# Performance work log

Measured on AMD Instinct MI355X. Metric: run time of the kernel, lower is better.

Reference implementation:

```python
import jax, jax.numpy as jnp
import numpy as np

B, L, A = 16, 32, 2046
M = A + 2  # user col + attributors + item col = 2048 nodes


def _xavier_uniform(key, shape, gain):
    fan_out, fan_in = shape  # torch 2D param: fan_in = shape[1], fan_out = shape[0]
    bound = gain * np.sqrt(6.0 / (fan_in + fan_out))
    return jax.random.uniform(key, shape, jnp.float32, -bound, bound)


def setup_inputs() -> dict:
    key = jax.random.key(0)
    k = jax.random.split(key, 7)
    user = jax.random.normal(k[0], (B, 6 * L, 1), jnp.float32)
    item = jax.random.normal(k[1], (B, 6 * L, 1), jnp.float32)
    attributor = jax.random.normal(k[2], (B, 6 * L, A), jnp.float32)
    adj = (jax.random.uniform(k[3], (M, M)) < 0.5).astype(jnp.float32)
    initial_weight = jax.random.normal(k[4], (M, M), jnp.float32)
    W_1 = _xavier_uniform(k[5], (6 * L, A), gain=np.sqrt(2.0))  # relu gain
    W_2 = _xavier_uniform(k[6], (6 * L, L), gain=1.44)
    return {"user": user, "item": item, "attributor": attributor,
            "adj": adj, "initial_weight": initial_weight,
            "W_1": W_1, "W_2": W_2}


def reference(user, item, attributor, adj, initial_weight, W_1, W_2):
    N = W_2.shape[1]  # = length L
    a = attributor * W_1                                   # (B, 6L, A)
    raw = jnp.concatenate([user, a, item], axis=2)         # (B, 6L, M)
    Q, K, V = jnp.split(raw, 3, axis=1)                    # each (B, 2L, M)
    r = jax.nn.relu
    # (relu(X).T @ W).T  ==  einsum over the 2L dim -> (B, L, M)
    Query = jnp.einsum('bnm,nl->blm', r(Q), W_2[:2 * N])
    Key = jnp.einsum('bnm,nl->blm', r(K), W_2[2 * N:4 * N])
    Value = jnp.einsum('bnm,nl->blm', r(V), W_2[4 * N:])
    # h = Query.mT @ Key * adj * initial_weight  -> (B, M, M)
    h = jnp.einsum('blm,bln->bmn', Query, Key) * adj * initial_weight
    d = h - jnp.swapaxes(h, -1, -2)
    exp_h = jnp.exp(jnp.where(d > 0, 0.0, d))              # exp(min(d, 0))
    causal = exp_h / (exp_h + jnp.swapaxes(exp_h, -1, -2)) * adj  # (B, M, M)
    Ans = Value @ causal                                    # (B, L, M)
    idx = jnp.array([0, Ans.shape[2] - 1])
    return Ans[:, :, idx]                                   # (B, L, 2)
```

## Files before the change

kernel.cpp:

```cpp
#include <hip/hip_runtime.h>
#include <math.h>

#define BB 16
#define LL 32
#define AA 2046
#define MM 2048
#define NROWS 192


__global__ __launch_bounds__(256) void prep_kernel(
    const float* __restrict__ user, const float* __restrict__ item,
    const float* __restrict__ W2, float* __restrict__ uv,
    float* __restrict__ bnd) {
  const int b = blockIdx.x, t = threadIdx.x;
  __shared__ float KQ[4][LL];
  __shared__ float uvs[4][64];
  if (t < 128) {
    const int q = t >> 5, l = t & 31;
    const float* __restrict__ src = (q & 1) ? item : user;
    const int rbase = (q < 2) ? 64 : 0;
    float acc = 0.f;
#pragma unroll
    for (int r = 0; r < 64; ++r)
      acc += fmaxf(src[b * NROWS + rbase + r], 0.f) * W2[(rbase + r) * LL + l];
    KQ[q][l] = acc;
  }
  __syncthreads();
  {
    const int which = t >> 6, r = t & 63;
    const int wrow = (which < 2) ? r : 64 + r;
    float acc = 0.f;
#pragma unroll
    for (int l = 0; l < LL; ++l) acc += W2[wrow * LL + l] * KQ[which][l];
    uvs[which][r] = acc;
    uv[which * (BB * 64) + b * 64 + r] = acc;
  }
  __syncthreads();
  if (t < 8) {
    const int which = t & 1, j = (t >> 1) & 1, stv = t >> 2;
    const float* __restrict__ src = which ? item : user;
    float acc = 0.f;
    if (stv == 0) {
#pragma unroll
      for (int r = 0; r < 64; ++r)
        acc += fmaxf(src[b * NROWS + r], 0.f) * uvs[j][r];
    } else {
#pragma unroll
      for (int r = 0; r < 64; ++r)
        acc += fmaxf(src[b * NROWS + 64 + r], 0.f) * uvs[2 + j][r];
    }
    bnd[((j * 2 + stv) * 2 + which) * BB + b] = acc;
  }
}

__global__ __launch_bounds__(256) void st_kernel(
    const float* __restrict__ att, const float* __restrict__ W1,
    const float* __restrict__ uv, float* __restrict__ part) {
  const int x = blockIdx.x, b = blockIdx.y, rc = blockIdx.z;
  const int t = threadIdx.x;
  const int z = rc >> 2;
  const int col0 = x * 512 + 2 * t;
  if (col0 >= AA) return;
  const float* __restrict__ w0 = uv + (2 * z) * (BB * 64) + b * 64;
  const float* __restrict__ w1 = uv + (2 * z + 1) * (BB * 64) + b * 64;
  const int r0 = rc * 16;
  const int wibase = r0 - z * 64;
  float a00 = 0.f, a01 = 0.f, a10 = 0.f, a11 = 0.f;
#pragma unroll
  for (int i = 0; i < 16; ++i) {
    const int r = r0 + i;
    const float2 av =
        ((const float2*)att)[((size_t)(b * NROWS + r) * AA + col0) >> 1];
    const float2 wv = ((const float2*)W1)[((size_t)r * AA + col0) >> 1];
    const float v0 = fmaxf(av.x * wv.x, 0.f);
    const float v1 = fmaxf(av.y * wv.y, 0.f);
    const float u0 = w0[wibase + i], u1 = w1[wibase + i];
    a00 += v0 * u0;
    a01 += v1 * u0;
    a10 += v0 * u1;
    a11 += v1 * u1;
  }
  float* p0 = part + ((size_t)(rc * 2 + 0) * BB + b) * 2048;
  float* p1 = part + ((size_t)(rc * 2 + 1) * BB + b) * 2048;
  ((float2*)p0)[col0 >> 1] = make_float2(a00, a01);
  ((float2*)p1)[col0 >> 1] = make_float2(a10, a11);
}

__global__ __launch_bounds__(256) void cweight_kernel(
    const float* __restrict__ adj, const float* __restrict__ iw,
    const float* __restrict__ part, const float* __restrict__ bnd,
    float* __restrict__ c) {
  const int idx = blockIdx.x * 256 + threadIdx.x;
  const int b = idx >> 11, n = idx & (MM - 1);
  float s0, s1, t0v, t1v;
  if (n == 0 || n == MM - 1) {
    const int which = (n == 0) ? 0 : 1;
    s0 = bnd[((0 * 2 + 0) * 2 + which) * BB + b];
    s1 = bnd[((1 * 2 + 0) * 2 + which) * BB + b];
    t0v = bnd[((0 * 2 + 1) * 2 + which) * BB + b];
    t1v = bnd[((1 * 2 + 1) * 2 + which) * BB + b];
  } else {
    const int col = n - 1;
    s0 = s1 = t0v = t1v = 0.f;
#pragma unroll
    for (int rc = 0; rc < 4; ++rc) {
      s0 += part[((size_t)(rc * 2 + 0) * BB + b) * 2048 + col];
      s1 += part[((size_t)(rc * 2 + 1) * BB + b) * 2048 + col];
      t0v += part[((size_t)((rc + 4) * 2 + 0) * BB + b) * 2048 + col];
      t1v += part[((size_t)((rc + 4) * 2 + 1) * BB + b) * 2048 + col];
    }
  }
  const float an0 = adj[(size_t)n * MM];
  const float an1 = adj[(size_t)n * MM + (MM - 1)];
  const float wn0 = an0 * iw[(size_t)n * MM];
  const float wn1 = an1 * iw[(size_t)n * MM + (MM - 1)];
  const float w0n = adj[n] * iw[n];
  const float w1n =
      adj[(size_t)(MM - 1) * MM + n] * iw[(size_t)(MM - 1) * MM + n];
  const float d0 = s0 * wn0 - t0v * w0n;
  const float d1 = s1 * wn1 - t1v * w1n;
  const float e0 = expf(-fabsf(d0));
  const float e1 = expf(-fabsf(d1));
  const float sig0 = (d0 > 0.f) ? 1.f / (1.f + e0) : e0 / (1.f + e0);
  const float sig1 = (d1 > 0.f) ? 1.f / (1.f + e1) : e1 / (1.f + e1);
  c[b * MM + n] = sig0 * an0;
  c[BB * MM + b * MM + n] = sig1 * an1;
}

__global__ __launch_bounds__(256) void gather_kernel(
    const float* __restrict__ user, const float* __restrict__ item,
    const float* __restrict__ att, const float* __restrict__ W1,
    const float* __restrict__ c, float* __restrict__ gg) {
  const int rv = blockIdx.x, b = blockIdx.y, t = threadIdx.x;
  const int r = 128 + rv;
  const int gr = b * NROWS + r;
  const float* __restrict__ c0 = c + b * MM;
  const float* __restrict__ c1 = c + BB * MM + b * MM;
  float g0 = 0.f, g1 = 0.f;
#pragma unroll
  for (int i = 0; i < 4; ++i) {
    const int col = i * 512 + 2 * t;
    if (col < AA) {
      const float2 av = ((const float2*)att)[((size_t)gr * AA + col) >> 1];
      const float2 wv = ((const float2*)W1)[((size_t)r * AA + col) >> 1];
      const float v0 = fmaxf(av.x * wv.x, 0.f);
      const float v1 = fmaxf(av.y * wv.y, 0.f);
      g0 += v0 * c0[col + 1] + v1 * c0[col + 2];
      g1 += v0 * c1[col + 1] + v1 * c1[col + 2];
    }
  }
  if (t == 0) {
    const float uval = fmaxf(user[gr], 0.f);
    const float ival = fmaxf(item[gr], 0.f);
    g0 += uval * c0[0] + ival * c0[MM - 1];
    g1 += uval * c1[0] + ival * c1[MM - 1];
  }
#pragma unroll
  for (int o = 32; o > 0; o >>= 1) {
    g0 += __shfl_down(g0, o);
    g1 += __shfl_down(g1, o);
  }
  __shared__ float rg[2][4];
  if ((t & 63) == 0) {
    rg[0][t >> 6] = g0;
    rg[1][t >> 6] = g1;
  }
  __syncthreads();
  if (t == 0) {
    const float s0 = rg[0][0] + rg[0][1] + rg[0][2] + rg[0][3];
    const float s1 = rg[1][0] + rg[1][1] + rg[1][2] + rg[1][3];
    ((float2*)gg)[b * 64 + rv] = make_float2(s0, s1);
  }
}

__global__ __launch_bounds__(64) void proj_kernel(
    const float* __restrict__ W2, const float* __restrict__ gg,
    float* __restrict__ out) {
  const int b = blockIdx.x, t = threadIdx.x;
  const int l = t & 31, j = t >> 5;
  float acc = 0.f;
#pragma unroll
  for (int i = 0; i < 64; ++i)
    acc += W2[(128 + i) * LL + l] * gg[(b * 64 + i) * 2 + j];
  out[b * 64 + l * 2 + j] = acc;
}

extern "C" void kernel_launch(void* const* d_in, const int* in_sizes, int n_in,
                              void* d_out, int out_size, void* d_ws,
                              size_t ws_size, hipStream_t stream) {
  const float* user = (const float*)d_in[0];
  const float* item = (const float*)d_in[1];
  const float* att = (const float*)d_in[2];
  const float* adj = (const float*)d_in[3];
  const float* iw = (const float*)d_in[4];
  const float* W1 = (const float*)d_in[5];
  const float* W2 = (const float*)d_in[6];
  float* out = (float*)d_out;

  float* uv = (float*)d_ws;
  float* bnd = uv + 4 * BB * 64;
  float* part = bnd + 128;
  float* c = part + 524288;
  float* gg = c + 2 * BB * MM;

  prep_kernel<<<dim3(BB), 256, 0, stream>>>(user, item, W2, uv, bnd);
  st_kernel<<<dim3(4, BB, 8), 256, 0, stream>>>(att, W1, uv, part);
  cweight_kernel<<<dim3(BB * MM / 256), 256, 0, stream>>>(adj, iw, part, bnd,
                                                          c);
  gather_kernel<<<dim3(64, BB), 256, 0, stream>>>(user, item, att, W1, c, gg);
  proj_kernel<<<dim3(BB), 64, 0, stream>>>(W2, gg, out);
}
```

Baseline: 113.8 us.

## Fuse partial-sum kernel with causal weight kernel via shared-memory reduction

Merges st_kernel and cweight_kernel into one kernel. Each block covers 64 columns, and four row-chunk groups reduce their partial sums through shared memory before computing the sigmoid weights. The two boundary nodes move to a tiny separate kernel. This removes the global partial buffer round trip and one launch. In exchange, loads become scalar rather than float2, the grid is smaller (512 blocks), and the epilogue runs on only 64 of 256 threads.

```diff
diff --git a/kernel.cpp b/kernel.cpp
--- a/kernel.cpp
+++ b/kernel.cpp
@@ -53,63 +53,47 @@
   }
 }
 
-__global__ __launch_bounds__(256) void st_kernel(
+__global__ __launch_bounds__(256) void stc2_kernel(
     const float* __restrict__ att, const float* __restrict__ W1,
-    const float* __restrict__ uv, float* __restrict__ part) {
-  const int x = blockIdx.x, b = blockIdx.y, rc = blockIdx.z;
-  const int t = threadIdx.x;
-  const int z = rc >> 2;
-  const int col0 = x * 512 + 2 * t;
-  if (col0 >= AA) return;
+    const float* __restrict__ uv, const float* __restrict__ adj,
+    const float* __restrict__ iw, const float* __restrict__ bnd,
+    float* __restrict__ c) {
+  const int x = blockIdx.x, b = blockIdx.y, t = threadIdx.x;
+  const int cl = t & 63;
+  const int q = t >> 6;
+  const int col = x * 64 + cl;
+  const int n = col + 1;
+  const int z = q >> 1;
+  const int r0 = q * 32;
+  const int wibase = r0 - z * 64;
+
   const float* __restrict__ w0 = uv + (2 * z) * (BB * 64) + b * 64;
   const float* __restrict__ w1 = uv + (2 * z + 1) * (BB * 64) + b * 64;
-  const int r0 = rc * 16;
-  const int wibase = r0 - z * 64;
-  float a00 = 0.f, a01 = 0.f, a10 = 0.f, a11 = 0.f;
-#pragma unroll
-  for (int i = 0; i < 16; ++i) {
-    const int r = r0 + i;
-    const float2 av =
-        ((const float2*)att)[((size_t)(b * NROWS + r) * AA + col0) >> 1];
-    const float2 wv = ((const float2*)W1)[((size_t)r * AA + col0) >> 1];
-    const float v0 = fmaxf(av.x * wv.x, 0.f);
-    const float v1 = fmaxf(av.y * wv.y, 0.f);
-    const float u0 = w0[wibase + i], u1 = w1[wibase + i];
-    a00 += v0 * u0;
-    a01 += v1 * u0;
-    a10 += v0 * u1;
-    a11 += v1 * u1;
-  }
-  float* p0 = part + ((size_t)(rc * 2 + 0) * BB + b) * 2048;
-  float* p1 = part + ((size_t)(rc * 2 + 1) * BB + b) * 2048;
-  ((float2*)p0)[col0 >> 1] = make_float2(a00, a01);
-  ((float2*)p1)[col0 >> 1] = make_float2(a10, a11);
-}
-
-__global__ __launch_bounds__(256) void cweight_kernel(
-    const float* __restrict__ adj, const float* __restrict__ iw,
-    const float* __restrict__ part, const float* __restrict__ bnd,
-    float* __restrict__ c) {
-  const int idx = blockIdx.x * 256 + threadIdx.x;
-  const int b = idx >> 11, n = idx & (MM - 1);
-  float s0, s1, t0v, t1v;
-  if (n == 0 || n == MM - 1) {
-    const int which = (n == 0) ? 0 : 1;
-    s0 = bnd[((0 * 2 + 0) * 2 + which) * BB + b];
-    s1 = bnd[((1 * 2 + 0) * 2 + which) * BB + b];
-    t0v = bnd[((0 * 2 + 1) * 2 + which) * BB + b];
-    t1v = bnd[((1 * 2 + 1) * 2 + which) * BB + b];
-  } else {
-    const int col = n - 1;
-    s0 = s1 = t0v = t1v = 0.f;
-#pragma unroll
-    for (int rc = 0; rc < 4; ++rc) {
-      s0 += part[((size_t)(rc * 2 + 0) * BB + b) * 2048 + col];
-      s1 += part[((size_t)(rc * 2 + 1) * BB + b) * 2048 + col];
-      t0v += part[((size_t)((rc + 4) * 2 + 0) * BB + b) * 2048 + col];
-      t1v += part[((size_t)((rc + 4) * 2 + 1) * BB + b) * 2048 + col];
+
+  float a0 = 0.f, a1 = 0.f;
+  if (col < AA) {
+#pragma unroll
+    for (int i = 0; i < 32; ++i) {
+      const int r = r0 + i;
+      const float v = fmaxf(att[(size_t)(b * NROWS + r) * AA + col] *
+                                W1[(size_t)r * AA + col],
+                            0.f);
+      a0 += v * w0[wibase + i];
+      a1 += v * w1[wibase + i];
     }
   }
+  __shared__ float red[4][2][64];
+  red[q][0][cl] = a0;
+  red[q][1][cl] = a1;
+  __syncthreads();
+  if (t >= 64) return;
+
+  float s0 = red[0][0][cl] + red[1][0][cl];
+  float s1 = red[0][1][cl] + red[1][1][cl];
+  float t0v = red[2][0][cl] + red[3][0][cl];
+  float t1v = red[2][1][cl] + red[3][1][cl];
+  if (col >= AA) return;
+
   const float an0 = adj[(size_t)n * MM];
   const float an1 = adj[(size_t)n * MM + (MM - 1)];
   const float wn0 = an0 * iw[(size_t)n * MM];
@@ -127,6 +111,34 @@
   c[BB * MM + b * MM + n] = sig1 * an1;
 }
 
+__global__ __launch_bounds__(64) void cbound_kernel(
+    const float* __restrict__ adj, const float* __restrict__ iw,
+    const float* __restrict__ bnd, float* __restrict__ c) {
+  const int t = threadIdx.x;
+  const int b = t >> 1, which = t & 1;
+  if (b >= BB) return;
+  const int n = which ? (MM - 1) : 0;
+  const float s0 = bnd[((0 * 2 + 0) * 2 + which) * BB + b];
+  const float s1 = bnd[((1 * 2 + 0) * 2 + which) * BB + b];
+  const float t0v = bnd[((0 * 2 + 1) * 2 + which) * BB + b];
+  const float t1v = bnd[((1 * 2 + 1) * 2 + which) * BB + b];
+  const float an0 = adj[(size_t)n * MM];
+  const float an1 = adj[(size_t)n * MM + (MM - 1)];
+  const float wn0 = an0 * iw[(size_t)n * MM];
+  const float wn1 = an1 * iw[(size_t)n * MM + (MM - 1)];
+  const float w0n = adj[n] * iw[n];
+  const float w1n =
+      adj[(size_t)(MM - 1) * MM + n] * iw[(size_t)(MM - 1) * MM + n];
+  const float d0 = s0 * wn0 - t0v * w0n;
+  const float d1 = s1 * wn1 - t1v * w1n;
+  const float e0 = expf(-fabsf(d0));
+  const float e1 = expf(-fabsf(d1));
+  const float sig0 = (d0 > 0.f) ? 1.f / (1.f + e0) : e0 / (1.f + e0);
+  const float sig1 = (d1 > 0.f) ? 1.f / (1.f + e1) : e1 / (1.f + e1);
+  c[b * MM + n] = sig0 * an0;
+  c[BB * MM + b * MM + n] = sig1 * an1;
+}
+
 __global__ __launch_bounds__(256) void gather_kernel(
     const float* __restrict__ user, const float* __restrict__ item,
     const float* __restrict__ att, const float* __restrict__ W1,
@@ -199,14 +211,12 @@
 
   float* uv = (float*)d_ws;
   float* bnd = uv + 4 * BB * 64;
-  float* part = bnd + 128;
-  float* c = part + 524288;
+  float* c = bnd + 128;
   float* gg = c + 2 * BB * MM;
 
   prep_kernel<<<dim3(BB), 256, 0, stream>>>(user, item, W2, uv, bnd);
-  st_kernel<<<dim3(4, BB, 8), 256, 0, stream>>>(att, W1, uv, part);
-  cweight_kernel<<<dim3(BB * MM / 256), 256, 0, stream>>>(adj, iw, part, bnd,
-                                                          c);
+  stc2_kernel<<<dim3(32, BB), 256, 0, stream>>>(att, W1, uv, adj, iw, bnd, c);
+  cbound_kernel<<<dim3(1), 64, 0, stream>>>(adj, iw, bnd, c);
   gather_kernel<<<dim3(64, BB), 256, 0, stream>>>(user, item, att, W1, c, gg);
   proj_kernel<<<dim3(BB), 64, 0, stream>>>(W2, gg, out);
 }
```

Result: slower. 125.2 us (+10.1%).
